# Kernel optimization log

Hardware: AMD Instinct MI355X
Metric: run time of the kernel (lower is better)

The kernel has to match this reference:

```python
import jax, jax.numpy as jnp
import numpy as np

NBINS = 51
BIN_WIDTH = 2.0 / (NBINS - 1)
BS, D = 1024, 128
N_CLASSES = 32


def setup_inputs() -> dict:
    key = jax.random.key(0)
    kx, kl = jax.random.split(key)
    x = jax.random.normal(kx, (BS, D), dtype=jnp.float32)
    x = x / jnp.linalg.norm(x, axis=1, keepdims=True)  # similarities in [-1, 1]
    labels = jax.random.randint(kl, (BS,), 0, N_CLASSES, dtype=jnp.int64)
    return {"x": x, "labels": labels}


def reference(x, labels):
    # Pairwise similarities of upper-triangular (i < j) pairs.
    sim = x @ x.T                                   # [bs, bs]
    bs = x.shape[0]
    iu, ju = jnp.triu_indices(bs, k=1)              # n_pairs indices
    s = sim[iu, ju]                                 # [n_pairs]
    pos = labels[iu] == labels[ju]                  # [n_pairs] bool

    # Soft (linear) binning: pair with sim s assigned bin value v = floor((s+1)/bw)*bw - 1
    # contributes (v+bw-s)/bw to bin b and (s-v)/bw to bin b+1 (triangular kernel),
    # exactly matching the original indsa/indsb masking scheme.
    b = jnp.floor((s + 1.0) / BIN_WIDTH).astype(jnp.int32)  # bin index in [0, nbins-1]
    v = b.astype(s.dtype) * BIN_WIDTH - 1.0                  # assigned bin value
    w_lo = (v + BIN_WIDTH - s) / BIN_WIDTH                   # weight for bin b
    w_hi = (s - v) / BIN_WIDTH                               # weight for bin b+1
    b_hi = jnp.clip(b + 1, 0, NBINS - 1)                     # w_hi == 0 when clipped

    def hist(mask):
        m = mask.astype(s.dtype)
        h = jnp.zeros((NBINS,), s.dtype)
        h = h.at[b].add(w_lo * m)
        h = h.at[b_hi].add(w_hi * m)
        return h / m.sum()

    hist_pos = hist(pos)
    hist_neg = hist(~pos)

    # CDF of positive histogram, then histogram loss.
    hist_pos_cdf = jnp.cumsum(hist_pos)
    return jnp.sum(hist_neg * hist_pos_cdf)
```

## Files before the change

kernel.cpp:

```cpp
#include <hip/hip_runtime.h>

#define NBINS 51
#define NT    32
#define TILE  32
#define DV4   32
#define NBLK  (NT * (NT + 1) / 2)
#define NCOPY 16
#define HSTR  103

__global__ __launch_bounds__(256) void pair_hist_kernel(
    const float* __restrict__ x,
    const int*   __restrict__ labels,
    float*       __restrict__ ghist)
{
    __shared__ float4 As[TILE][DV4];
    __shared__ float4 Bs[TILE][DV4];
    __shared__ int    la[TILE], lb[TILE];
    __shared__ float  shist[NCOPY * HSTR];

    int rem = blockIdx.x;
    int bi = 0;
    while (rem >= NT - bi) { rem -= NT - bi; ++bi; }
    const int bj = bi + rem;

    const int t = threadIdx.x;
    for (int k = t; k < NCOPY * HSTR; k += 256) shist[k] = 0.0f;

    const float4* xv = (const float4*)x;
    #pragma unroll
    for (int k = 0; k < 4; ++k) {
        int e = t + 256 * k;
        int r = e >> 5;
        int c = e & 31;
        int sw = c ^ ((r >> 1) & 7);
        As[r][sw] = xv[(bi * TILE + r) * DV4 + c];
        Bs[r][sw] = xv[(bj * TILE + r) * DV4 + c];
    }
    if (t < TILE) {
        la[t] = labels[bi * TILE + t];
        lb[t] = labels[bj * TILE + t];
    }
    __syncthreads();

    const int tx = t & 15;
    const int ty = t >> 4;
    const int i0 = ty * 2, j0 = tx * 2;
    const int kA = ty & 7;
    const int kB = tx & 7;

    float acc00 = 0.f, acc01 = 0.f, acc10 = 0.f, acc11 = 0.f;
    #pragma unroll 4
    for (int d4 = 0; d4 < DV4; ++d4) {
        float4 a0 = As[i0    ][d4 ^ kA];
        float4 a1 = As[i0 + 1][d4 ^ kA];
        float4 b0 = Bs[j0    ][d4 ^ kB];
        float4 b1 = Bs[j0 + 1][d4 ^ kB];
        acc00 += a0.x*b0.x + a0.y*b0.y + a0.z*b0.z + a0.w*b0.w;
        acc01 += a0.x*b1.x + a0.y*b1.y + a0.z*b1.z + a0.w*b1.w;
        acc10 += a1.x*b0.x + a1.y*b0.y + a1.z*b0.z + a1.w*b0.w;
        acc11 += a1.x*b1.x + a1.y*b1.y + a1.z*b1.z + a1.w*b1.w;
    }

    const float BW = 2.0f / (NBINS - 1);
    float accs[2][2] = {{acc00, acc01}, {acc10, acc11}};
    float* myh = &shist[(t & (NCOPY - 1)) * HSTR];

    #pragma unroll
    for (int r = 0; r < 2; ++r) {
        #pragma unroll
        for (int c = 0; c < 2; ++c) {
            int gi = bi * TILE + i0 + r;
            int gj = bj * TILE + j0 + c;
            if (gi < gj) {
                float s = accs[r][c];
                int b = (int)floorf((s + 1.0f) / BW);
                b = min(max(b, 0), NBINS - 1);
                float v = (float)b * BW - 1.0f;
                float wlo = (v + BW - s) / BW;
                float whi = (s - v) / BW;
                int bh = min(b + 1, NBINS - 1);
                int base = (la[i0 + r] == lb[j0 + c]) ? 0 : NBINS;
                unsafeAtomicAdd(&myh[base + b],  wlo);
                unsafeAtomicAdd(&myh[base + bh], whi);
            }
        }
    }

    __syncthreads();
    if (t < 2 * NBINS) {
        float s = 0.f;
        #pragma unroll
        for (int c = 0; c < NCOPY; ++c) s += shist[c * HSTR + t];
        unsafeAtomicAdd(&ghist[t], s);
    }
}

__global__ void finalize_kernel(const float* __restrict__ gh,
                                float* __restrict__ out)
{
    int t = threadIdx.x;
    float hp = (t < NBINS) ? gh[t]         : 0.0f;
    float hn = (t < NBINS) ? gh[NBINS + t] : 0.0f;

    float sp = hp, sn = hn;
    #pragma unroll
    for (int off = 32; off > 0; off >>= 1) {
        sp += __shfl_xor(sp, off, 64);
        sn += __shfl_xor(sn, off, 64);
    }

    float cdf = hp;
    #pragma unroll
    for (int off = 1; off < 64; off <<= 1) {
        float v = __shfl_up(cdf, off, 64);
        if (t >= off) cdf += v;
    }

    float contrib = hn * cdf;
    #pragma unroll
    for (int off = 32; off > 0; off >>= 1)
        contrib += __shfl_xor(contrib, off, 64);

    if (t == 0) out[0] = contrib / (sp * sn);
}

extern "C" void kernel_launch(void* const* d_in, const int* in_sizes, int n_in,
                              void* d_out, int out_size, void* d_ws, size_t ws_size,
                              hipStream_t stream)
{
    const float* x      = (const float*)d_in[0];
    const int*   labels = (const int*)d_in[1];
    float*       ghist  = (float*)d_ws;

    hipMemsetAsync(ghist, 0, 2 * NBINS * sizeof(float), stream);
    pair_hist_kernel<<<NBLK, 256, 0, stream>>>(x, labels, ghist);
    finalize_kernel<<<1, 64, 0, stream>>>(ghist, (float*)d_out);
}
```

Before: 79.47 us.

## Use 16x16 single-wave tiles with direct global loads and split global histograms

```diff
diff --git a/kernel.cpp b/kernel.cpp
--- a/kernel.cpp
+++ b/kernel.cpp
@@ -1,65 +1,58 @@
 #include <hip/hip_runtime.h>
 
 #define NBINS 51
-#define NT    32
-#define TILE  32
+#define NTT   64
+#define TILE  16
 #define DV4   32
-#define NBLK  (NT * (NT + 1) / 2)
+#define NBLK  (NTT * (NTT + 1) / 2)
 #define NCOPY 16
 #define HSTR  103
+#define NSPLIT 8
 
-__global__ __launch_bounds__(256) void pair_hist_kernel(
+__global__ __launch_bounds__(64, 4) void pair_hist_kernel(
     const float* __restrict__ x,
     const int*   __restrict__ labels,
     float*       __restrict__ ghist)
 {
-    __shared__ float4 As[TILE][DV4];
-    __shared__ float4 Bs[TILE][DV4];
-    __shared__ int    la[TILE], lb[TILE];
-    __shared__ float  shist[NCOPY * HSTR];
+    __shared__ float shist[NCOPY * HSTR];
 
     int rem = blockIdx.x;
     int bi = 0;
-    while (rem >= NT - bi) { rem -= NT - bi; ++bi; }
+    while (rem >= NTT - bi) { rem -= NTT - bi; ++bi; }
     const int bj = bi + rem;
 
     const int t = threadIdx.x;
-    for (int k = t; k < NCOPY * HSTR; k += 256) shist[k] = 0.0f;
+    for (int k = t; k < NCOPY * HSTR; k += 64) shist[k] = 0.0f;
 
-    const float4* xv = (const float4*)x;
-    #pragma unroll
-    for (int k = 0; k < 4; ++k) {
-        int e = t + 256 * k;
-        int r = e >> 5;
-        int c = e & 31;
-        int sw = c ^ ((r >> 1) & 7);
-        As[r][sw] = xv[(bi * TILE + r) * DV4 + c];
-        Bs[r][sw] = xv[(bj * TILE + r) * DV4 + c];
-    }
-    if (t < TILE) {
-        la[t] = labels[bi * TILE + t];
-        lb[t] = labels[bj * TILE + t];
-    }
-    __syncthreads();
+    const int tx = t & 7;
+    const int ty = t >> 3;
+    const int gi0 = bi * TILE + ty * 2;
+    const int gj0 = bj * TILE + tx * 2;
 
-    const int tx = t & 15;
-    const int ty = t >> 4;
-    const int i0 = ty * 2, j0 = tx * 2;
-    const int kA = ty & 7;
-    const int kB = tx & 7;
+    const float4* a0p = (const float4*)(x + (size_t)gi0 * 128);
+    const float4* a1p = a0p + DV4;
+    const float4* b0p = (const float4*)(x + (size_t)gj0 * 128);
+    const float4* b1p = b0p + DV4;
 
     float acc00 = 0.f, acc01 = 0.f, acc10 = 0.f, acc11 = 0.f;
     #pragma unroll 4
-    for (int d4 = 0; d4 < DV4; ++d4) {
-        float4 a0 = As[i0    ][d4 ^ kA];
-        float4 a1 = As[i0 + 1][d4 ^ kA];
-        float4 b0 = Bs[j0    ][d4 ^ kB];
-        float4 b1 = Bs[j0 + 1][d4 ^ kB];
+    for (int d = 0; d < DV4; ++d) {
+        float4 a0 = a0p[d];
+        float4 a1 = a1p[d];
+        float4 b0 = b0p[d];
+        float4 b1 = b1p[d];
         acc00 += a0.x*b0.x + a0.y*b0.y + a0.z*b0.z + a0.w*b0.w;
         acc01 += a0.x*b1.x + a0.y*b1.y + a0.z*b1.z + a0.w*b1.w;
         acc10 += a1.x*b0.x + a1.y*b0.y + a1.z*b0.z + a1.w*b0.w;
         acc11 += a1.x*b1.x + a1.y*b1.y + a1.z*b1.z + a1.w*b1.w;
     }
+
+    const int la0 = labels[gi0], la1 = labels[gi0 + 1];
+    const int lb0 = labels[gj0], lb1 = labels[gj0 + 1];
+    const int las[2] = {la0, la1};
+    const int lbs[2] = {lb0, lb1};
+
+    __syncthreads();
 
     const float BW = 2.0f / (NBINS - 1);
     float accs[2][2] = {{acc00, acc01}, {acc10, acc11}};
@@ -69,8 +62,8 @@
     for (int r = 0; r < 2; ++r) {
         #pragma unroll
         for (int c = 0; c < 2; ++c) {
-            int gi = bi * TILE + i0 + r;
-            int gj = bj * TILE + j0 + c;
+            int gi = gi0 + r;
+            int gj = gj0 + c;
             if (gi < gj) {
                 float s = accs[r][c];
                 int b = (int)floorf((s + 1.0f) / BW);
@@ -79,7 +72,7 @@
                 float wlo = (v + BW - s) / BW;
                 float whi = (s - v) / BW;
                 int bh = min(b + 1, NBINS - 1);
-                int base = (la[i0 + r] == lb[j0 + c]) ? 0 : NBINS;
+                int base = (las[r] == lbs[c]) ? 0 : NBINS;
                 unsafeAtomicAdd(&myh[base + b],  wlo);
                 unsafeAtomicAdd(&myh[base + bh], whi);
             }
@@ -87,11 +80,12 @@
     }
 
     __syncthreads();
-    if (t < 2 * NBINS) {
+    float* gh = ghist + (blockIdx.x & (NSPLIT - 1)) * (2 * NBINS);
+    for (int bin = t; bin < 2 * NBINS; bin += 64) {
         float s = 0.f;
         #pragma unroll
-        for (int c = 0; c < NCOPY; ++c) s += shist[c * HSTR + t];
-        unsafeAtomicAdd(&ghist[t], s);
+        for (int c = 0; c < NCOPY; ++c) s += shist[c * HSTR + bin];
+        if (s != 0.0f) unsafeAtomicAdd(&gh[bin], s);
     }
 }
 
@@ -99,8 +93,14 @@
                                 float* __restrict__ out)
 {
     int t = threadIdx.x;
-    float hp = (t < NBINS) ? gh[t]         : 0.0f;
-    float hn = (t < NBINS) ? gh[NBINS + t] : 0.0f;
+    float hp = 0.f, hn = 0.f;
+    if (t < NBINS) {
+        #pragma unroll
+        for (int c = 0; c < NSPLIT; ++c) {
+            hp += gh[c * (2 * NBINS) + t];
+            hn += gh[c * (2 * NBINS) + NBINS + t];
+        }
+    }
 
     float sp = hp, sn = hn;
     #pragma unroll
@@ -132,7 +132,7 @@
     const int*   labels = (const int*)d_in[1];
     float*       ghist  = (float*)d_ws;
 
-    hipMemsetAsync(ghist, 0, 2 * NBINS * sizeof(float), stream);
-    pair_hist_kernel<<<NBLK, 256, 0, stream>>>(x, labels, ghist);
+    hipMemsetAsync(ghist, 0, NSPLIT * 2 * NBINS * sizeof(float), stream);
+    pair_hist_kernel<<<NBLK, 64, 0, stream>>>(x, labels, ghist);
     finalize_kernel<<<1, 64, 0, stream>>>(ghist, (float*)d_out);
 }
```

New measurement: 85.35 us. 7.4% more time.
